# Performance work log

Hardware: AMD Instinct MI355X
Metric: run time of the kernel (lower is better)

## Reference

```python
import jax, jax.numpy as jnp
import numpy as np

NUM_RAYS = 65536
N_COARSE = 64
INTERS_FINE = 128


def setup_inputs() -> dict:
    key = jax.random.key(0)
    k1, k2, k3 = jax.random.split(key, 3)
    weights = jax.random.uniform(k1, (NUM_RAYS, N_COARSE), dtype=jnp.float32)
    # sorted bin edges in [2, 6), turned into contiguous intervals [start, end]
    t_edges = jnp.sort(2.0 + 4.0 * jax.random.uniform(k2, (NUM_RAYS, N_COARSE + 1), dtype=jnp.float32), axis=-1)
    t_inters = jnp.stack([t_edges[:, :-1], t_edges[:, 1:]], axis=-1)  # [R, N, 2]
    # stratified jittered u, exactly as the original np.random construction
    eps32 = np.finfo(np.float32).eps
    s = 1.0 / (INTERS_FINE + 1)
    base = jnp.arange(INTERS_FINE + 1, dtype=jnp.float32) * s  # [F+1]
    jitter = jax.random.uniform(k3, (NUM_RAYS, INTERS_FINE + 1), dtype=jnp.float32,
                                minval=0.0, maxval=s - eps32)
    u = jnp.minimum(base[None, :] + jitter, 1.0 - eps32)
    return {"weights": weights, "t_inters": t_inters, "u": u}


def reference(weights, t_inters, u):
    eps = 1e-05
    num_rays = weights.shape[0]
    # maxblur of weights (mip-NeRF style) + floor
    wp = jnp.concatenate([weights[:, :1], weights, weights[:, -1:]], axis=-1)
    wmax = jnp.maximum(wp[:, :-1], wp[:, 1:])
    w = (wmax[:, :-1] + wmax[:, 1:]) * 0.5 + 0.01  # [R, N]
    # bin edges
    t_vals = jnp.concatenate([t_inters[..., 0], t_inters[:, -1:, 1]], axis=-1)  # [R, N+1]
    # normalize to pdf with eps padding
    wsum = jnp.sum(w, axis=-1, keepdims=True)
    padding = jnp.maximum(0.0, eps - wsum)
    w = w + padding / w.shape[-1]
    wsum = wsum + padding
    pdf = w / wsum
    cdf = jnp.minimum(1.0, jnp.cumsum(pdf[..., :-1], axis=-1))
    cdf = jnp.concatenate([jnp.zeros((num_rays, 1), jnp.float32), cdf,
                           jnp.ones((num_rays, 1), jnp.float32)], axis=-1)  # [R, N+1]
    # inverse CDF: the original's broadcast mask + max/min reductions are exactly
    # searchsorted(cdf, u, side='right'); idx-1 = last bin with cdf <= u (since
    # cdf[:,0]=0 <= u and u < 1 = cdf[:,-1], indices are always interior).
    idx = jax.vmap(lambda c, uu: jnp.searchsorted(c, uu, side='right'))(cdf, u)  # [R, F+1]
    last = cdf.shape[-1] - 1
    i0 = jnp.clip(idx - 1, 0, last)
    i1 = jnp.clip(idx, 0, last)
    cdf_g0 = jnp.take_along_axis(cdf, i0, axis=-1)
    cdf_g1 = jnp.take_along_axis(cdf, i1, axis=-1)
    bins_g0 = jnp.take_along_axis(t_vals, i0, axis=-1)
    bins_g1 = jnp.take_along_axis(t_vals, i1, axis=-1)
    t = (u - cdf_g0) / (cdf_g1 - cdf_g0)
    t = jnp.where(jnp.isnan(t), 0.0, t)  # matches t[t != t] = 0
    t = jnp.clip(t, 0.0, 1.0)
    samples = bins_g0 + t * (bins_g1 - bins_g0)  # [R, F+1]
    samples = jax.lax.stop_gradient(samples)     # matches .detach()
    samples = jnp.sort(samples, axis=-1)
    return jnp.stack([samples[:, :-1], samples[:, 1:]], axis=-1)  # [R, F, 2]
```

## Files before the change

### kernel.cpp

```cpp
#include <hip/hip_runtime.h>


#define RAYS_PER_BLOCK 8
#define DPP_WAVE_SHL1 0x130
#define DPP_WAVE_SHR1 0x138

typedef float fvec4 __attribute__((ext_vector_type(4)));

template <int CTRL, int ROW_MASK>
__device__ __forceinline__ float dpp_add(float x) {
    int sh = __builtin_amdgcn_update_dpp(0, __float_as_int(x), CTRL, ROW_MASK, 0xf, false);
    return x + __int_as_float(sh);
}

template <int CTRL>
__device__ __forceinline__ float dpp_old_f(float old, float src) {
    return __int_as_float(__builtin_amdgcn_update_dpp(
        __float_as_int(old), __float_as_int(src), CTRL, 0xf, 0xf, false));
}

__device__ __forceinline__ float readlane_f(float v, int lane) {
    return __int_as_float(__builtin_amdgcn_readlane(__float_as_int(v), lane));
}

__device__ __forceinline__ float bperm(int byteaddr, float v) {
    return __int_as_float(__builtin_amdgcn_ds_bpermute(byteaddr, __float_as_int(v)));
}

__device__ __forceinline__ int search6(float uu, float cdfv,
                                       float c8, float c16, float c24, float c32,
                                       float c40, float c48, float c56) {
    bool g1 = (c32 <= uu);
    int loB = g1 ? 128 : 0;
    float cA = g1 ? c48 : c16;
    bool g2 = (cA <= uu);
    loB += g2 ? 64 : 0;
    float pL = g1 ? c40 : c8;
    float pH = g1 ? c56 : c24;
    float cB = g2 ? pH : pL;
    loB += (cB <= uu) ? 32 : 0;
    float c = bperm(loB + 12, cdfv);
    loB += (c <= uu) ? 16 : 0;
    c = bperm(loB + 4, cdfv);
    loB += (c <= uu) ? 8 : 0;
    c = bperm(loB, cdfv);
    loB += (c <= uu) ? 4 : 0;
    return loB;
}

__global__ __launch_bounds__(64 * RAYS_PER_BLOCK)
void sample_pdf_kernel(const float* __restrict__ weights,
                       const float* __restrict__ t_inters,
                       const float* __restrict__ u,
                       float* __restrict__ out,
                       int R) {
    const int lane = threadIdx.x & 63;
    const int wave = threadIdx.x >> 6;
    const int ray  = blockIdx.x * RAYS_PER_BLOCK + wave;
    if (ray >= R) return;

    float  w  = weights[(long)ray * 64 + lane];
    float2 ti = ((const float2*)t_inters)[(long)ray * 64 + lane];
    const float* ub = u + (long)ray * 129;
    float u0 = ub[2 * lane];
    float u1 = ub[2 * lane + 1];
    float u2 = ub[128];

    float wm1 = dpp_old_f<DPP_WAVE_SHR1>(w, w);
    float wp1 = dpp_old_f<DPP_WAVE_SHL1>(w, w);
    float w2 = (fmaxf(wm1, w) + fmaxf(w, wp1)) * 0.5f + 0.01f;

    float scan = w2;
    scan = dpp_add<0x111, 0xf>(scan);
    scan = dpp_add<0x112, 0xf>(scan);
    scan = dpp_add<0x114, 0xf>(scan);
    scan = dpp_add<0x118, 0xf>(scan);
    scan = dpp_add<0x142, 0xa>(scan);
    scan = dpp_add<0x143, 0xc>(scan);

    float wsum = readlane_f(scan, 63);
    float cdfv = fminf(1.0f, scan * __builtin_amdgcn_rcpf(wsum));
    if (lane == 63) cdfv = 1.0f;

    float clo = dpp_old_f<DPP_WAVE_SHR1>(0.0f, cdfv);
    float nx  = dpp_old_f<DPP_WAVE_SHL1>(ti.y, ti.x);
    float dt  = nx - ti.x;
    float Bv  = dt * __builtin_amdgcn_rcpf(cdfv - clo);
    float Av  = ti.x - clo * Bv;

    float c8  = readlane_f(cdfv, 7),  c16 = readlane_f(cdfv, 15);
    float c24 = readlane_f(cdfv, 23), c32 = readlane_f(cdfv, 31);
    float c40 = readlane_f(cdfv, 39), c48 = readlane_f(cdfv, 47);
    float c56 = readlane_f(cdfv, 55);

    int lA = search6(u0, cdfv, c8, c16, c24, c32, c40, c48, c56);
    int lB = search6(u1, cdfv, c8, c16, c24, c32, c40, c48, c56);
    float s_a = bperm(lA, Av) + bperm(lA, Bv) * u0;
    float s_b = bperm(lB, Av) + bperm(lB, Bv) * u1;

    unsigned long long mask = __ballot(cdfv <= u2);
    int p = __popcll(mask);
    float s2 = readlane_f(Av, p) + readlane_f(Bv, p) * u2;

    float s_an = dpp_old_f<DPP_WAVE_SHL1>(s2, s_a);

    fvec4 o4 = { s_a, s_b, s_b, s_an };
    __builtin_nontemporal_store(o4, &((fvec4*)out)[(long)ray * 64 + lane]);
}

extern "C" void kernel_launch(void* const* d_in, const int* in_sizes, int n_in,
                              void* d_out, int out_size, void* d_ws, size_t ws_size,
                              hipStream_t stream) {
    const float* weights  = (const float*)d_in[0];
    const float* t_inters = (const float*)d_in[1];
    const float* u        = (const float*)d_in[2];
    float* out            = (float*)d_out;

    const int R = in_sizes[0] / 64;
    const int grid = (R + RAYS_PER_BLOCK - 1) / RAYS_PER_BLOCK;
    sample_pdf_kernel<<<grid, 64 * RAYS_PER_BLOCK, 0, stream>>>(weights, t_inters, u, out, R);
}
```

Measured before the change: 28.06 us.

## Process eight rays per wave with software-prefetched next-ray loads

```diff
diff --git a/kernel.cpp b/kernel.cpp
--- a/kernel.cpp
+++ b/kernel.cpp
@@ -1,7 +1,8 @@
 #include <hip/hip_runtime.h>
 
 
-#define RAYS_PER_BLOCK 8
+#define WAVES_PER_BLOCK 4
+#define RAYS_PER_WAVE 8
 #define DPP_WAVE_SHL1 0x130
 #define DPP_WAVE_SHR1 0x138
 
@@ -48,7 +49,7 @@
     return loB;
 }
 
-__global__ __launch_bounds__(64 * RAYS_PER_BLOCK)
+__global__ __launch_bounds__(64 * WAVES_PER_BLOCK)
 void sample_pdf_kernel(const float* __restrict__ weights,
                        const float* __restrict__ t_inters,
                        const float* __restrict__ u,
@@ -56,56 +57,73 @@
                        int R) {
     const int lane = threadIdx.x & 63;
     const int wave = threadIdx.x >> 6;
-    const int ray  = blockIdx.x * RAYS_PER_BLOCK + wave;
-    if (ray >= R) return;
+    const int ray0 = (blockIdx.x * WAVES_PER_BLOCK + wave) * RAYS_PER_WAVE;
 
-    float  w  = weights[(long)ray * 64 + lane];
-    float2 ti = ((const float2*)t_inters)[(long)ray * 64 + lane];
-    const float* ub = u + (long)ray * 129;
-    float u0 = ub[2 * lane];
-    float u1 = ub[2 * lane + 1];
-    float u2 = ub[128];
+    float  w_n  = weights[(long)ray0 * 64 + lane];
+    float2 ti_n = ((const float2*)t_inters)[(long)ray0 * 64 + lane];
+    const float* ub_n = u + (long)ray0 * 129;
+    float u0_n = ub_n[2 * lane];
+    float u1_n = ub_n[2 * lane + 1];
+    float u2_n = ub_n[128];
 
-    float wm1 = dpp_old_f<DPP_WAVE_SHR1>(w, w);
-    float wp1 = dpp_old_f<DPP_WAVE_SHL1>(w, w);
-    float w2 = (fmaxf(wm1, w) + fmaxf(w, wp1)) * 0.5f + 0.01f;
+    #pragma unroll
+    for (int i = 0; i < RAYS_PER_WAVE; ++i) {
+        const int ray = ray0 + i;
+        float  w  = w_n;
+        float2 ti = ti_n;
+        float  u0 = u0_n, u1 = u1_n, u2 = u2_n;
 
-    float scan = w2;
-    scan = dpp_add<0x111, 0xf>(scan);
-    scan = dpp_add<0x112, 0xf>(scan);
-    scan = dpp_add<0x114, 0xf>(scan);
-    scan = dpp_add<0x118, 0xf>(scan);
-    scan = dpp_add<0x142, 0xa>(scan);
-    scan = dpp_add<0x143, 0xc>(scan);
+        if (i + 1 < RAYS_PER_WAVE) {
+            const int rn = ray + 1;
+            w_n  = weights[(long)rn * 64 + lane];
+            ti_n = ((const float2*)t_inters)[(long)rn * 64 + lane];
+            const float* ub = u + (long)rn * 129;
+            u0_n = ub[2 * lane];
+            u1_n = ub[2 * lane + 1];
+            u2_n = ub[128];
+        }
 
-    float wsum = readlane_f(scan, 63);
-    float cdfv = fminf(1.0f, scan * __builtin_amdgcn_rcpf(wsum));
-    if (lane == 63) cdfv = 1.0f;
+        float wm1 = dpp_old_f<DPP_WAVE_SHR1>(w, w);
+        float wp1 = dpp_old_f<DPP_WAVE_SHL1>(w, w);
+        float w2 = (fmaxf(wm1, w) + fmaxf(w, wp1)) * 0.5f + 0.01f;
 
-    float clo = dpp_old_f<DPP_WAVE_SHR1>(0.0f, cdfv);
-    float nx  = dpp_old_f<DPP_WAVE_SHL1>(ti.y, ti.x);
-    float dt  = nx - ti.x;
-    float Bv  = dt * __builtin_amdgcn_rcpf(cdfv - clo);
-    float Av  = ti.x - clo * Bv;
+        float scan = w2;
+        scan = dpp_add<0x111, 0xf>(scan);
+        scan = dpp_add<0x112, 0xf>(scan);
+        scan = dpp_add<0x114, 0xf>(scan);
+        scan = dpp_add<0x118, 0xf>(scan);
+        scan = dpp_add<0x142, 0xa>(scan);
+        scan = dpp_add<0x143, 0xc>(scan);
 
-    float c8  = readlane_f(cdfv, 7),  c16 = readlane_f(cdfv, 15);
-    float c24 = readlane_f(cdfv, 23), c32 = readlane_f(cdfv, 31);
-    float c40 = readlane_f(cdfv, 39), c48 = readlane_f(cdfv, 47);
-    float c56 = readlane_f(cdfv, 55);
+        float wsum = readlane_f(scan, 63);
+        float cdfv = scan * __builtin_amdgcn_rcpf(wsum);
+        if (lane == 63) cdfv = 1.0f;
 
-    int lA = search6(u0, cdfv, c8, c16, c24, c32, c40, c48, c56);
-    int lB = search6(u1, cdfv, c8, c16, c24, c32, c40, c48, c56);
-    float s_a = bperm(lA, Av) + bperm(lA, Bv) * u0;
-    float s_b = bperm(lB, Av) + bperm(lB, Bv) * u1;
+        float clo = dpp_old_f<DPP_WAVE_SHR1>(0.0f, cdfv);
+        float nx  = dpp_old_f<DPP_WAVE_SHL1>(ti.y, ti.x);
+        float dt  = nx - ti.x;
+        float Bv  = dt * __builtin_amdgcn_rcpf(cdfv - clo);
+        float Av  = ti.x - clo * Bv;
 
-    unsigned long long mask = __ballot(cdfv <= u2);
-    int p = __popcll(mask);
-    float s2 = readlane_f(Av, p) + readlane_f(Bv, p) * u2;
+        unsigned long long mask = __ballot(cdfv <= u2);
+        int p = __popcll(mask);
+        float s2 = readlane_f(Av, p) + readlane_f(Bv, p) * u2;
 
-    float s_an = dpp_old_f<DPP_WAVE_SHL1>(s2, s_a);
+        float c8  = readlane_f(cdfv, 7),  c16 = readlane_f(cdfv, 15);
+        float c24 = readlane_f(cdfv, 23), c32 = readlane_f(cdfv, 31);
+        float c40 = readlane_f(cdfv, 39), c48 = readlane_f(cdfv, 47);
+        float c56 = readlane_f(cdfv, 55);
 
-    fvec4 o4 = { s_a, s_b, s_b, s_an };
-    __builtin_nontemporal_store(o4, &((fvec4*)out)[(long)ray * 64 + lane]);
+        int lA = search6(u0, cdfv, c8, c16, c24, c32, c40, c48, c56);
+        int lB = search6(u1, cdfv, c8, c16, c24, c32, c40, c48, c56);
+        float s_a = bperm(lA, Av) + bperm(lA, Bv) * u0;
+        float s_b = bperm(lB, Av) + bperm(lB, Bv) * u1;
+
+        float s_an = dpp_old_f<DPP_WAVE_SHL1>(s2, s_a);
+
+        fvec4 o4 = { s_a, s_b, s_b, s_an };
+        __builtin_nontemporal_store(o4, &((fvec4*)out)[(long)ray * 64 + lane]);
+    }
 }
 
 extern "C" void kernel_launch(void* const* d_in, const int* in_sizes, int n_in,
@@ -117,6 +135,7 @@
     float* out            = (float*)d_out;
 
     const int R = in_sizes[0] / 64;
-    const int grid = (R + RAYS_PER_BLOCK - 1) / RAYS_PER_BLOCK;
-    sample_pdf_kernel<<<grid, 64 * RAYS_PER_BLOCK, 0, stream>>>(weights, t_inters, u, out, R);
+    const int rays_per_block = WAVES_PER_BLOCK * RAYS_PER_WAVE;
+    const int grid = (R + rays_per_block - 1) / rays_per_block;
+    sample_pdf_kernel<<<grid, 64 * WAVES_PER_BLOCK, 0, stream>>>(weights, t_inters, u, out, R);
 }
```

New measurement: 29.65 us. +5.7%, slower.
